# Kernel optimization log

Hardware: AMD Instinct MI355X
Metric: run time of the kernel (lower is better)

Reference implementation:

```python
import jax, jax.numpy as jnp
import numpy as np

NUM_HEADS = 16
DIM_EMBED = 1024
DIM_CROSS = 768
DIM_HEAD = DIM_EMBED // NUM_HEADS


def setup_inputs() -> dict:
    key = jax.random.key(0)
    ks = jax.random.split(key, 10)
    B, Sq, Skv = 16, 4096, 77
    s_e = 1.0 / np.sqrt(DIM_EMBED)
    s_c = 1.0 / np.sqrt(DIM_CROSS)
    return {
        "x": jax.random.normal(ks[0], (B, Sq, DIM_EMBED), jnp.float32),
        "y": jax.random.normal(ks[1], (B, Skv, DIM_CROSS), jnp.float32),
        "wq": jax.random.uniform(ks[2], (DIM_EMBED, DIM_EMBED), jnp.float32, -s_e, s_e),
        "bq": jax.random.uniform(ks[3], (DIM_EMBED,), jnp.float32, -s_e, s_e),
        "wk": jax.random.uniform(ks[4], (DIM_CROSS, DIM_EMBED), jnp.float32, -s_c, s_c),
        "bk": jax.random.uniform(ks[5], (DIM_EMBED,), jnp.float32, -s_c, s_c),
        "wv": jax.random.uniform(ks[6], (DIM_CROSS, DIM_EMBED), jnp.float32, -s_c, s_c),
        "bv": jax.random.uniform(ks[7], (DIM_EMBED,), jnp.float32, -s_c, s_c),
        "wo": jax.random.uniform(ks[8], (DIM_EMBED, DIM_EMBED), jnp.float32, -s_e, s_e),
        "bo": jax.random.uniform(ks[9], (DIM_EMBED,), jnp.float32, -s_e, s_e),
    }


def reference(x, y, wq, bq, wk, bk, wv, bv, wo, bo):
    B, Sq, E = x.shape
    H, D = NUM_HEADS, DIM_HEAD
    q = (x @ wq + bq).reshape(B, Sq, H, D).transpose(0, 2, 1, 3)   # [B,H,Sq,D]
    k = (y @ wk + bk).reshape(B, -1, H, D).transpose(0, 2, 1, 3)   # [B,H,Skv,D]
    v = (y @ wv + bv).reshape(B, -1, H, D).transpose(0, 2, 1, 3)   # [B,H,Skv,D]
    scale = 1.0 / jnp.sqrt(jnp.asarray(D, dtype=q.dtype))
    scores = jnp.einsum("bhqd,bhkd->bhqk", q, k) * scale           # [B,H,Sq,Skv]
    attn = jax.nn.softmax(scores, axis=-1)
    out = jnp.einsum("bhqk,bhkd->bhqd", attn, v)                   # [B,H,Sq,D]
    out = out.transpose(0, 2, 1, 3).reshape(B, Sq, E)
    return out @ wo + bo
```

## Files before the change

kernel.cpp:

```cpp
#include <hip/hip_runtime.h>

typedef unsigned short u16;
typedef __attribute__((ext_vector_type(4))) float f32x4;
typedef __attribute__((ext_vector_type(8))) short bf16x8;
typedef __attribute__((ext_vector_type(8))) unsigned short u16x8;
typedef __attribute__((ext_vector_type(4))) unsigned short u16x4;

__device__ __forceinline__ u16 f2bf(float f) {
  union { float f; unsigned u; } v; v.f = f;
  unsigned r = v.u + 0x7FFFu + ((v.u >> 16) & 1u);
  return (u16)(r >> 16);
}
__device__ __forceinline__ float bf2f(u16 h) {
  union { unsigned u; float f; } v; v.u = ((unsigned)h) << 16; return v.f;
}

__device__ __forceinline__ void gload_lds16(const void* g, void* l) {
  __builtin_amdgcn_global_load_lds((const __attribute__((address_space(1))) void*)g,
                                   (__attribute__((address_space(3))) void*)l, 16, 0, 0);
}


__global__ void k_zero(u16x8* __restrict__ p, int n8) {
  int i = blockIdx.x * blockDim.x + threadIdx.x;
  int stride = gridDim.x * blockDim.x;
  u16x8 z = (u16x8)0;
  for (; i < n8; i += stride) p[i] = z;
}

__global__ void k_cvt_x(const float* __restrict__ in, u16* __restrict__ out, int n4) {
  int i = blockIdx.x * blockDim.x + threadIdx.x;
  int stride = gridDim.x * blockDim.x;
  const f32x4* in4 = (const f32x4*)in;
  u16x4* out4 = (u16x4*)out;
  for (; i < n4; i += stride) {
    f32x4 v = in4[i];
    u16x4 o;
    o[0] = f2bf(v[0]); o[1] = f2bf(v[1]); o[2] = f2bf(v[2]); o[3] = f2bf(v[3]);
    out4[i] = o;
  }
}

__global__ void k_prep_wt(const float* __restrict__ wq, const float* __restrict__ wo,
                          const float* __restrict__ wk, const float* __restrict__ wv,
                          u16* __restrict__ WQ1T, u16* __restrict__ WO1T,
                          u16* __restrict__ WK1T, u16* __restrict__ WV1T) {
  __shared__ u16 tile[64][72];
  int bid = blockIdx.x;
  const float* w; u16* o; int K;
  if (bid < 256)      { w = wq; o = WQ1T; K = 1024; }
  else if (bid < 512) { w = wo; o = WO1T; K = 1024; bid -= 256; }
  else if (bid < 704) { w = wk; o = WK1T; K = 768;  bid -= 512; }
  else                { w = wv; o = WV1T; K = 768;  bid -= 704; }
  const int ti = bid >> 4, tj = bid & 15;
  const int t = threadIdx.x;
  const int r = t >> 2, cq = (t & 3) * 16;

  const float* src = w + (size_t)(ti * 64 + r) * 1024 + tj * 64 + cq;
#pragma unroll
  for (int j4 = 0; j4 < 4; ++j4) {
    f32x4 v = *(const f32x4*)(src + j4 * 4);
#pragma unroll
    for (int e = 0; e < 4; ++e) tile[r][cq + j4 * 4 + e] = f2bf(v[e]);
  }
  __syncthreads();

  u16 vals[16];
#pragma unroll
  for (int j = 0; j < 16; ++j) vals[j] = tile[cq + j][r];
  u16* dst = o + (size_t)(tj * 64 + r) * K + ti * 64 + cq;
  *(u16x8*)dst = *(u16x8*)&vals[0];
  *(u16x8*)(dst + 8) = *(u16x8*)&vals[8];
}

__global__ void k_prep_y(const float* __restrict__ y, u16* __restrict__ yb, int n4) {
  int i = blockIdx.x * blockDim.x + threadIdx.x;
  int stride = gridDim.x * blockDim.x;
  const f32x4* in4 = (const f32x4*)y;
  u16x4* out4 = (u16x4*)yb;
  for (; i < n4; i += stride) {
    f32x4 v = in4[i];
    u16x4 o;
    o[0] = f2bf(v[0]); o[1] = f2bf(v[1]); o[2] = f2bf(v[2]); o[3] = f2bf(v[3]);
    out4[i] = o;
  }
}

__global__ __launch_bounds__(256, 2) void k_gemm_kv(
    const u16* __restrict__ A,
    const u16* __restrict__ BK1, const float* __restrict__ bkb, u16* __restrict__ KTo,
    const u16* __restrict__ BV1, const float* __restrict__ bvb, u16* __restrict__ VTo)
{
  const int M = 1232, Kdim = 768;
  __shared__ u16 sA[128 * 32];
  __shared__ u16 sB[128 * 32];
  const int t = threadIdx.x;
  const int half = blockIdx.x >= 80;
  const int bb = blockIdx.x - half * 80;
  const u16* B = half ? BV1 : BK1;
  const float* bias = half ? bvb : bkb;
  u16* outp = half ? VTo : KTo;
  const int bm = bb / 8, bn = bb % 8;
  const int m0 = bm * 128, n0 = bn * 128;
  const int l = t & 63, wv_ = t >> 6;
  const int lr = l & 15, lg = l >> 4;
  const int wm = (wv_ >> 1) * 64, wn = (wv_ & 1) * 64;

  const int srow = t >> 2;
  const int ssw = ((t >> 2) & 3) ^ ((t >> 4) & 3);
  const int scol = ((t & 3) ^ ssw) * 8;
  char* ldsA = (char*)sA;
  char* ldsB = (char*)sB;
  const int ldsoff = wv_ * 1024;

  const int swl = (lr & 3) ^ ((lr >> 2) & 3);
  const int rds = (lg ^ swl) * 8;

  f32x4 acc[4][4] = {};

  for (int kt = 0; kt < Kdim / 32; ++kt) {
    const int k0 = kt * 32;
    __syncthreads();
    {
      int r1 = m0 + srow;       if (r1 > M - 1) r1 = M - 1;
      int r2 = m0 + 64 + srow;  if (r2 > M - 1) r2 = M - 1;
      gload_lds16(A + (size_t)r1 * Kdim + k0 + scol, ldsA + 0    + ldsoff);
      gload_lds16(A + (size_t)r2 * Kdim + k0 + scol, ldsA + 4096 + ldsoff);
      gload_lds16(B + (size_t)(n0 + srow) * Kdim + k0 + scol,      ldsB + 0    + ldsoff);
      gload_lds16(B + (size_t)(n0 + 64 + srow) * Kdim + k0 + scol, ldsB + 4096 + ldsoff);
    }
    __syncthreads();
    bf16x8 af[4], bfr[4];
#pragma unroll
    for (int mt = 0; mt < 4; ++mt)
      af[mt] = *(const bf16x8*)&sA[(wm + mt * 16 + lr) * 32 + rds];
#pragma unroll
    for (int nt = 0; nt < 4; ++nt)
      bfr[nt] = *(const bf16x8*)&sB[(wn + nt * 16 + lr) * 32 + rds];
#pragma unroll
    for (int mt = 0; mt < 4; ++mt)
#pragma unroll
      for (int nt = 0; nt < 4; ++nt)
        acc[mt][nt] = __builtin_amdgcn_mfma_f32_16x16x32_bf16(af[mt], bfr[nt], acc[mt][nt], 0, 0, 0);
  }

#pragma unroll
  for (int mt = 0; mt < 4; ++mt) {
#pragma unroll
    for (int nt = 0; nt < 4; ++nt) {
      const int gc = n0 + wn + nt * 16 + lr;
      const float bb2 = bias[gc];
#pragma unroll
      for (int r = 0; r < 4; ++r) {
        const int gr = m0 + wm + mt * 16 + lg * 4 + r;
        const float v = acc[mt][nt][r] + bb2;
        if (gr < M) {
          int bI = gr / 77, s = gr - bI * 77;
          int hh = gc >> 6, d = gc & 63;
          if (!half)
            outp[(((size_t)bI * 16 + hh) * 96 + s) * 64 + d] = f2bf(v);
          else
            outp[(((size_t)bI * 16 + hh) * 64 + d) * 96 + s] = f2bf(v);
        }
      }
    }
  }
}

template <int EPI>
__global__ __launch_bounds__(512, 2) void gemm256(
    const u16* __restrict__ A, const u16* __restrict__ Bp,
    const float* __restrict__ bias, void* __restrict__ outp,
    const u16* __restrict__ KT, const u16* __restrict__ VT)
{
  __shared__ char lds[131072];
  const int t = threadIdx.x;
  const int cpx = (int)gridDim.x >> 3;
  const int swz = ((int)blockIdx.x & 7) * cpx + ((int)blockIdx.x >> 3);
  const int bm = swz >> 2, bn = swz & 3;
  const int m0 = bm * 256, n0 = bn * 256;
  const int w = t >> 6, l = t & 63, lr = l & 15, lg = l >> 4;
  const int wm = w >> 2, wn = w & 3;

  const int srow = t >> 2;
  const int scol = ((t & 3) ^ ((t >> 2) & 3) ^ ((t >> 4) & 3)) * 8;
  const int rsw = (lg ^ (lr & 3) ^ ((lr >> 2) & 3)) << 4;
  const int arow = wm * 128 + lr;
  const int brow = wn * 64 + lr;

  f32x4 acc[8][4] = {};

#define RD(dstA, dstB, sbb) { \
  _Pragma("unroll") for (int q = 0; q < 8; ++q) \
    dstA[q] = *(const bf16x8*)(lds + (sbb) + ((arow + q * 16) << 6) + rsw); \
  _Pragma("unroll") for (int nt = 0; nt < 4; ++nt) \
    dstB[nt] = *(const bf16x8*)(lds + (sbb) + 16384 + ((brow + nt * 16) << 6) + rsw); }
#define STAGE(kt, sbb) { \
    gload_lds16(A  + (size_t)(m0 + srow) * 1024 + (kt) * 32 + scol,       lds + (sbb) + t * 16); \
    gload_lds16(A  + (size_t)(m0 + 128 + srow) * 1024 + (kt) * 32 + scol, lds + (sbb) + 8192 + t * 16); \
    gload_lds16(Bp + (size_t)(n0 + srow) * 1024 + (kt) * 32 + scol,       lds + (sbb) + 16384 + t * 16); \
    gload_lds16(Bp + (size_t)(n0 + 128 + srow) * 1024 + (kt) * 32 + scol, lds + (sbb) + 24576 + t * 16); }
#define MM(a_, b_) { __builtin_amdgcn_s_setprio(1); \
  _Pragma("unroll") for (int q = 0; q < 8; ++q) \
    _Pragma("unroll") for (int nt = 0; nt < 4; ++nt) \
      acc[q][nt] = __builtin_amdgcn_mfma_f32_16x16x32_bf16(a_[q], b_[nt], acc[q][nt], 0, 0, 0); \
  __builtin_amdgcn_s_setprio(0); }
#define BAR __builtin_amdgcn_s_barrier()
#define SB0 __builtin_amdgcn_sched_barrier(0)
#define VM8 asm volatile("s_waitcnt vmcnt(8)" ::: "memory")

  bf16x8 aA[8], bA[4], aB[8], bB[4];

  STAGE(0, 0); STAGE(1, 32768); STAGE(2, 65536);
  VM8; SB0; BAR;
  RD(aA, bA, 0);

  int rdo = 32768, sto = 98304;
#pragma unroll 1
  for (int tt = 0; tt < 32; tt += 2) {
    {
      int ks = tt + 3; if (ks > 31) ks = 31;
      STAGE(ks, sto); sto = (sto + 32768) & 131071;
      VM8; SB0; BAR;
      RD(aB, bB, rdo); rdo = (rdo + 32768) & 131071;
      MM(aA, bA);
      BAR;
    }
    {
      int ks = tt + 4; if (ks > 31) ks = 31;
      STAGE(ks, sto); sto = (sto + 32768) & 131071;
      VM8; SB0; BAR;
      RD(aA, bA, rdo); rdo = (rdo + 32768) & 131071;
      MM(aB, bB);
      BAR;
    }
  }
  asm volatile("s_waitcnt vmcnt(0)" ::: "memory");
  SB0; BAR;

#undef RD
#undef STAGE
#undef MM
#undef BAR
#undef SB0
#undef VM8

  if constexpr (EPI == 1) {
#pragma unroll
    for (int q = 0; q < 8; ++q) {
#pragma unroll
      for (int nt = 0; nt < 4; ++nt) {
        const int gc = n0 + wn * 64 + nt * 16 + lr;
        const float bb = bias[gc];
#pragma unroll
        for (int r = 0; r < 4; ++r) {
          const int gr = m0 + wm * 128 + q * 16 + lg * 4 + r;
          ((float*)outp)[(size_t)gr * 1024 + gc] = acc[q][nt][r] + bb;
        }
      }
    }
  } else {
    const int hh = (n0 >> 6) + wn;
    const int b = m0 >> 12;
    const u16* gK = KT + (size_t)(b * 16 + hh) * (96 * 64);
    const u16* gV = VT + (size_t)(b * 16 + hh) * (64 * 96);
    u16* Qs = (u16*)(lds + w * 16384);
    u16* Ps = (u16*)(lds + w * 16384 + 8192);
    u16* QBo = (u16*)outp;

    float bb[4];
#pragma unroll
    for (int nt = 0; nt < 4; ++nt) bb[nt] = bias[n0 + wn * 64 + nt * 16 + lr];

#pragma unroll
    for (int cc = 0; cc < 4; ++cc) {
#pragma unroll
      for (int qq = 0; qq < 2; ++qq)
#pragma unroll
        for (int nt = 0; nt < 4; ++nt)
#pragma unroll
          for (int r = 0; r < 4; ++r)
            Qs[(qq * 16 + lg * 4 + r) * 72 + nt * 16 + lr] =
                f2bf(acc[cc * 2 + qq][nt][r] + bb[nt]);

      bf16x8 aq[2][2];
#pragma unroll
      for (int qq = 0; qq < 2; ++qq)
#pragma unroll
        for (int ks = 0; ks < 2; ++ks)
          aq[qq][ks] = *(const bf16x8*)&Qs[(qq * 16 + lr) * 72 + ks * 32 + lg * 8];

      f32x4 s_[2][5] = {};
#pragma unroll
      for (int nt = 0; nt < 5; ++nt) {
#pragma unroll
        for (int ks = 0; ks < 2; ++ks) {
          bf16x8 bk = *(const bf16x8*)&gK[(nt * 16 + lr) * 64 + ks * 32 + lg * 8];
#pragma unroll
          for (int qq = 0; qq < 2; ++qq)
            s_[qq][nt] = __builtin_amdgcn_mfma_f32_16x16x32_bf16(aq[qq][ks], bk, s_[qq][nt], 0, 0, 0);
        }
      }
#pragma unroll
      for (int qq = 0; qq < 2; ++qq)
#pragma unroll
        for (int nt = 0; nt < 5; ++nt)
#pragma unroll
          for (int r = 0; r < 4; ++r)
            s_[qq][nt][r] *= 0.125f;
      if (lr >= 13) {
#pragma unroll
        for (int qq = 0; qq < 2; ++qq)
#pragma unroll
          for (int r = 0; r < 4; ++r)
            s_[qq][4][r] = -1e30f;
      }

      float ri[2][4];
#pragma unroll
      for (int qq = 0; qq < 2; ++qq) {
#pragma unroll
        for (int r = 0; r < 4; ++r) {
          float m1 = s_[qq][0][r];
#pragma unroll
          for (int nt = 1; nt < 5; ++nt) m1 = fmaxf(m1, s_[qq][nt][r]);
          m1 = fmaxf(m1, __shfl_xor(m1, 1, 64));
          m1 = fmaxf(m1, __shfl_xor(m1, 2, 64));
          m1 = fmaxf(m1, __shfl_xor(m1, 4, 64));
          m1 = fmaxf(m1, __shfl_xor(m1, 8, 64));
          float s1 = 0.f;
#pragma unroll
          for (int nt = 0; nt < 5; ++nt) {
            float e = __expf(s_[qq][nt][r] - m1);
            s_[qq][nt][r] = e;
            s1 += e;
          }
          s1 += __shfl_xor(s1, 1, 64);
          s1 += __shfl_xor(s1, 2, 64);
          s1 += __shfl_xor(s1, 4, 64);
          s1 += __shfl_xor(s1, 8, 64);
          ri[qq][r] = 1.0f / s1;
        }
      }

#pragma unroll
      for (int qq = 0; qq < 2; ++qq)
#pragma unroll
        for (int nt = 0; nt < 5; ++nt)
#pragma unroll
          for (int r = 0; r < 4; ++r)
            Ps[(qq * 16 + lg * 4 + r) * 104 + nt * 16 + lr] = f2bf(s_[qq][nt][r] * ri[qq][r]);
#pragma unroll
      for (int qq = 0; qq < 2; ++qq)
#pragma unroll
        for (int r = 0; r < 4; ++r)
          Ps[(qq * 16 + lg * 4 + r) * 104 + 80 + lr] = 0;

      f32x4 o_[2][4] = {};
#pragma unroll
      for (int ks = 0; ks < 3; ++ks) {
        bf16x8 ap[2];
#pragma unroll
        for (int qq = 0; qq < 2; ++qq)
          ap[qq] = *(const bf16x8*)&Ps[(qq * 16 + lr) * 104 + ks * 32 + lg * 8];
#pragma unroll
        for (int nt = 0; nt < 4; ++nt) {
          bf16x8 bv = *(const bf16x8*)&gV[(nt * 16 + lr) * 96 + ks * 32 + lg * 8];
#pragma unroll
          for (int qq = 0; qq < 2; ++qq)
            o_[qq][nt] = __builtin_amdgcn_mfma_f32_16x16x32_bf16(ap[qq], bv, o_[qq][nt], 0, 0, 0);
        }
      }

#pragma unroll
      for (int qq = 0; qq < 2; ++qq)
#pragma unroll
        for (int nt = 0; nt < 4; ++nt)
#pragma unroll
          for (int r = 0; r < 4; ++r)
            QBo[(size_t)(m0 + wm * 128 + cc * 32 + qq * 16 + lg * 4 + r) * 1024
                + hh * 64 + nt * 16 + lr] = f2bf(o_[qq][nt][r]);
    }
  }
}


extern "C" void kernel_launch(void* const* d_in, const int* in_sizes, int n_in,
                              void* d_out, int out_size, void* d_ws, size_t ws_size,
                              hipStream_t stream) {
  const float* x  = (const float*)d_in[0];
  const float* y  = (const float*)d_in[1];
  const float* wq = (const float*)d_in[2];
  const float* bq = (const float*)d_in[3];
  const float* wk = (const float*)d_in[4];
  const float* bk = (const float*)d_in[5];
  const float* wv = (const float*)d_in[6];
  const float* bv = (const float*)d_in[7];
  const float* wo = (const float*)d_in[8];
  const float* bo = (const float*)d_in[9];

  char* ws = (char*)d_ws;
  u16* QB   = (u16*)(ws + 0);
  u16* WQ1T = (u16*)(ws + 134217728);
  u16* WO1T = (u16*)(ws + 136314880);
  u16* WK1T = (u16*)(ws + 138412032);
  u16* WV1T = (u16*)(ws + 139984896);
  u16* YB   = (u16*)(ws + 141557760);
  u16* KT   = (u16*)(ws + 143654912);
  u16* VT   = (u16*)(ws + 146800640);

  u16*   XB  = (u16*)d_out;
  float* OUT = (float*)d_out;

  k_zero<<<768, 256, 0, stream>>>((u16x8*)KT, 393216);
  k_cvt_x<<<4096, 256, 0, stream>>>(x, XB, 16777216);
  k_prep_wt<<<896, 256, 0, stream>>>(wq, wo, wk, wv, WQ1T, WO1T, WK1T, WV1T);
  k_prep_y<<<924, 256, 0, stream>>>(y, YB, 236544);

  k_gemm_kv<<<160, 256, 0, stream>>>(YB, WK1T, bk, KT, WV1T, bv, VT);

  gemm256<0><<<1024, 512, 0, stream>>>(XB, WQ1T, bq, QB, KT, VT);

  gemm256<1><<<1024, 512, 0, stream>>>(QB, WO1T, bo, OUT, nullptr, nullptr);
}
```

Before: 533.6 us.

## Retile GEMM to 256x128 blocks with BK=64 and preload K/V fragments

Changes the main GEMM tile from 256x256 with K-step 32 to 256x128 with K-step 64. The pipeline becomes three 48KB LDS stages with an 8-way XOR swizzle, and the grid doubles to 2048 blocks. In the fused attention epilogue, K and V fragments are loaded into registers once per warp instead of inside the loops. The 144KB of LDS likely allows only one block per CU despite launch_bounds(512,2), and the smaller N tile lowers arithmetic intensity per block.

```diff
diff --git a/kernel.cpp b/kernel.cpp
--- a/kernel.cpp
+++ b/kernel.cpp
@@ -173,64 +173,72 @@
     const float* __restrict__ bias, void* __restrict__ outp,
     const u16* __restrict__ KT, const u16* __restrict__ VT)
 {
-  __shared__ char lds[131072];
+  __shared__ char lds[147456];
   const int t = threadIdx.x;
   const int cpx = (int)gridDim.x >> 3;
   const int swz = ((int)blockIdx.x & 7) * cpx + ((int)blockIdx.x >> 3);
-  const int bm = swz >> 2, bn = swz & 3;
-  const int m0 = bm * 256, n0 = bn * 256;
+  const int bm = swz >> 3, bn = swz & 7;
+  const int m0 = bm * 256, n0 = bn * 128;
   const int w = t >> 6, l = t & 63, lr = l & 15, lg = l >> 4;
-  const int wm = w >> 2, wn = w & 3;
-
-  const int srow = t >> 2;
-  const int scol = ((t & 3) ^ ((t >> 2) & 3) ^ ((t >> 4) & 3)) * 8;
-  const int rsw = (lg ^ (lr & 3) ^ ((lr >> 2) & 3)) << 4;
-  const int arow = wm * 128 + lr;
+  const int wm = w >> 1, wn = w & 1;
+  const int wbase = w * 1024;
+
+  const int srow = t >> 3;
+  const int scol = ((t & 7) ^ (srow & 7)) << 3;
+  const int sw16_0 = ((lg) ^ (lr & 7)) << 4;
+  const int sw16_1 = ((4 + lg) ^ (lr & 7)) << 4;
+  const int arow = wm * 64 + lr;
   const int brow = wn * 64 + lr;
 
-  f32x4 acc[8][4] = {};
-
-#define RD(dstA, dstB, sbb) { \
-  _Pragma("unroll") for (int q = 0; q < 8; ++q) \
-    dstA[q] = *(const bf16x8*)(lds + (sbb) + ((arow + q * 16) << 6) + rsw); \
-  _Pragma("unroll") for (int nt = 0; nt < 4; ++nt) \
-    dstB[nt] = *(const bf16x8*)(lds + (sbb) + 16384 + ((brow + nt * 16) << 6) + rsw); }
+  f32x4 acc[4][4] = {};
+
+#define RD(dstA, dstB, rbb) { \
+  _Pragma("unroll") for (int q = 0; q < 4; ++q) { \
+    dstA[q]     = *(const bf16x8*)(lds + (rbb) + ((arow + q * 16) << 7) + sw16_0); \
+    dstA[4 + q] = *(const bf16x8*)(lds + (rbb) + ((arow + q * 16) << 7) + sw16_1); } \
+  _Pragma("unroll") for (int nt = 0; nt < 4; ++nt) { \
+    dstB[nt]     = *(const bf16x8*)(lds + (rbb) + 32768 + ((brow + nt * 16) << 7) + sw16_0); \
+    dstB[4 + nt] = *(const bf16x8*)(lds + (rbb) + 32768 + ((brow + nt * 16) << 7) + sw16_1); } }
 #define STAGE(kt, sbb) { \
-    gload_lds16(A  + (size_t)(m0 + srow) * 1024 + (kt) * 32 + scol,       lds + (sbb) + t * 16); \
-    gload_lds16(A  + (size_t)(m0 + 128 + srow) * 1024 + (kt) * 32 + scol, lds + (sbb) + 8192 + t * 16); \
-    gload_lds16(Bp + (size_t)(n0 + srow) * 1024 + (kt) * 32 + scol,       lds + (sbb) + 16384 + t * 16); \
-    gload_lds16(Bp + (size_t)(n0 + 128 + srow) * 1024 + (kt) * 32 + scol, lds + (sbb) + 24576 + t * 16); }
+  _Pragma("unroll") for (int j = 0; j < 4; ++j) \
+    gload_lds16(A + (size_t)(m0 + j * 64 + srow) * 1024 + (kt) * 64 + scol, \
+                lds + (sbb) + j * 8192 + wbase); \
+  _Pragma("unroll") for (int j = 0; j < 2; ++j) \
+    gload_lds16(Bp + (size_t)(n0 + j * 64 + srow) * 1024 + (kt) * 64 + scol, \
+                lds + (sbb) + 32768 + j * 8192 + wbase); }
 #define MM(a_, b_) { __builtin_amdgcn_s_setprio(1); \
-  _Pragma("unroll") for (int q = 0; q < 8; ++q) \
-    _Pragma("unroll") for (int nt = 0; nt < 4; ++nt) \
-      acc[q][nt] = __builtin_amdgcn_mfma_f32_16x16x32_bf16(a_[q], b_[nt], acc[q][nt], 0, 0, 0); \
+  _Pragma("unroll") for (int kk = 0; kk < 2; ++kk) \
+    _Pragma("unroll") for (int q = 0; q < 4; ++q) \
+      _Pragma("unroll") for (int nt = 0; nt < 4; ++nt) \
+        acc[q][nt] = __builtin_amdgcn_mfma_f32_16x16x32_bf16(a_[kk * 4 + q], b_[kk * 4 + nt], acc[q][nt], 0, 0, 0); \
   __builtin_amdgcn_s_setprio(0); }
 #define BAR __builtin_amdgcn_s_barrier()
 #define SB0 __builtin_amdgcn_sched_barrier(0)
-#define VM8 asm volatile("s_waitcnt vmcnt(8)" ::: "memory")
-
-  bf16x8 aA[8], bA[4], aB[8], bB[4];
-
-  STAGE(0, 0); STAGE(1, 32768); STAGE(2, 65536);
-  VM8; SB0; BAR;
+#define VM6 asm volatile("s_waitcnt vmcnt(6)" ::: "memory")
+
+  bf16x8 aA[8], bA[8], aB[8], bB[8];
+
+  STAGE(0, 0);
+  STAGE(1, 49152);
+  VM6; SB0; BAR;
   RD(aA, bA, 0);
 
-  int rdo = 32768, sto = 98304;
+  int rdo = 49152, sto = 2 * 49152;
 #pragma unroll 1
-  for (int tt = 0; tt < 32; tt += 2) {
+  for (int i = 0; i < 16; i += 2) {
     {
-      int ks = tt + 3; if (ks > 31) ks = 31;
-      STAGE(ks, sto); sto = (sto + 32768) & 131071;
-      VM8; SB0; BAR;
-      RD(aB, bB, rdo); rdo = (rdo + 32768) & 131071;
+      int ks = i + 2; if (ks > 15) ks = 15;
+      STAGE(ks, sto); sto += 49152; if (sto == 147456) sto = 0;
+      VM6; SB0; BAR;
+      RD(aB, bB, rdo); rdo += 49152; if (rdo == 147456) rdo = 0;
       MM(aA, bA);
       BAR;
     }
     {
-      int ks = tt + 4; if (ks > 31) ks = 31;
-      STAGE(ks, sto); sto = (sto + 32768) & 131071;
-      VM8; SB0; BAR;
-      RD(aA, bA, rdo); rdo = (rdo + 32768) & 131071;
+      int ks = i + 3; if (ks > 15) ks = 15;
+      STAGE(ks, sto); sto += 49152; if (sto == 147456) sto = 0;
+      VM6; SB0; BAR;
+      RD(aA, bA, rdo); rdo += 49152; if (rdo == 147456) rdo = 0;
       MM(aB, bB);
       BAR;
     }
@@ -243,18 +251,18 @@
 #undef MM
 #undef BAR
 #undef SB0
-#undef VM8
+#undef VM6
 
   if constexpr (EPI == 1) {
 #pragma unroll
-    for (int q = 0; q < 8; ++q) {
+    for (int q = 0; q < 4; ++q) {
 #pragma unroll
       for (int nt = 0; nt < 4; ++nt) {
         const int gc = n0 + wn * 64 + nt * 16 + lr;
         const float bb = bias[gc];
 #pragma unroll
         for (int r = 0; r < 4; ++r) {
-          const int gr = m0 + wm * 128 + q * 16 + lg * 4 + r;
+          const int gr = m0 + wm * 64 + q * 16 + lg * 4 + r;
           ((float*)outp)[(size_t)gr * 1024 + gc] = acc[q][nt][r] + bb;
         }
       }
@@ -268,12 +276,24 @@
     u16* Ps = (u16*)(lds + w * 16384 + 8192);
     u16* QBo = (u16*)outp;
 
+    bf16x8 fk[5][2], fv[4][3];
+#pragma unroll
+    for (int nt = 0; nt < 5; ++nt)
+#pragma unroll
+      for (int ks = 0; ks < 2; ++ks)
+        fk[nt][ks] = *(const bf16x8*)&gK[(nt * 16 + lr) * 64 + ks * 32 + lg * 8];
+#pragma unroll
+    for (int nt = 0; nt < 4; ++nt)
+#pragma unroll
+      for (int ks = 0; ks < 3; ++ks)
+        fv[nt][ks] = *(const bf16x8*)&gV[(nt * 16 + lr) * 96 + ks * 32 + lg * 8];
+
     float bb[4];
 #pragma unroll
     for (int nt = 0; nt < 4; ++nt) bb[nt] = bias[n0 + wn * 64 + nt * 16 + lr];
 
 #pragma unroll
-    for (int cc = 0; cc < 4; ++cc) {
+    for (int cc = 0; cc < 2; ++cc) {
 #pragma unroll
       for (int qq = 0; qq < 2; ++qq)
 #pragma unroll
@@ -292,15 +312,12 @@
 
       f32x4 s_[2][5] = {};
 #pragma unroll
-      for (int nt = 0; nt < 5; ++nt) {
-#pragma unroll
-        for (int ks = 0; ks < 2; ++ks) {
-          bf16x8 bk = *(const bf16x8*)&gK[(nt * 16 + lr) * 64 + ks * 32 + lg * 8];
+      for (int nt = 0; nt < 5; ++nt)
+#pragma unroll
+        for (int ks = 0; ks < 2; ++ks)
 #pragma unroll
           for (int qq = 0; qq < 2; ++qq)
-            s_[qq][nt] = __builtin_amdgcn_mfma_f32_16x16x32_bf16(aq[qq][ks], bk, s_[qq][nt], 0, 0, 0);
-        }
-      }
+            s_[qq][nt] = __builtin_amdgcn_mfma_f32_16x16x32_bf16(aq[qq][ks], fk[nt][ks], s_[qq][nt], 0, 0, 0);
 #pragma unroll
       for (int qq = 0; qq < 2; ++qq)
 #pragma unroll
@@ -364,12 +381,10 @@
         for (int qq = 0; qq < 2; ++qq)
           ap[qq] = *(const bf16x8*)&Ps[(qq * 16 + lr) * 104 + ks * 32 + lg * 8];
 #pragma unroll
-        for (int nt = 0; nt < 4; ++nt) {
-          bf16x8 bv = *(const bf16x8*)&gV[(nt * 16 + lr) * 96 + ks * 32 + lg * 8];
+        for (int nt = 0; nt < 4; ++nt)
 #pragma unroll
           for (int qq = 0; qq < 2; ++qq)
-            o_[qq][nt] = __builtin_amdgcn_mfma_f32_16x16x32_bf16(ap[qq], bv, o_[qq][nt], 0, 0, 0);
-        }
+            o_[qq][nt] = __builtin_amdgcn_mfma_f32_16x16x32_bf16(ap[qq], fv[nt][ks], o_[qq][nt], 0, 0, 0);
       }
 
 #pragma unroll
@@ -378,7 +393,7 @@
         for (int nt = 0; nt < 4; ++nt)
 #pragma unroll
           for (int r = 0; r < 4; ++r)
-            QBo[(size_t)(m0 + wm * 128 + cc * 32 + qq * 16 + lg * 4 + r) * 1024
+            QBo[(size_t)(m0 + wm * 64 + cc * 32 + qq * 16 + lg * 4 + r) * 1024
                 + hh * 64 + nt * 16 + lr] = f2bf(o_[qq][nt][r]);
     }
   }
@@ -419,7 +434,7 @@
 
   k_gemm_kv<<<160, 256, 0, stream>>>(YB, WK1T, bk, KT, WV1T, bv, VT);
 
-  gemm256<0><<<1024, 512, 0, stream>>>(XB, WQ1T, bq, QB, KT, VT);
-
-  gemm256<1><<<1024, 512, 0, stream>>>(QB, WO1T, bo, OUT, nullptr, nullptr);
-}
+  gemm256<0><<<2048, 512, 0, stream>>>(XB, WQ1T, bq, QB, KT, VT);
+
+  gemm256<1><<<2048, 512, 0, stream>>>(QB, WO1T, bo, OUT, nullptr, nullptr);
+}
```

After: 561.0 us. 5.1% more time.
